# Optimization experiments

Measured on AMD Instinct MI355X. Metric: run time of the kernel, lower is better.

The kernel has to match this reference:

```python
import jax, jax.numpy as jnp
from jax import lax
import numpy as np

START = 1  # strings_utils.SpecialSymbol.START
B, T, H, V = 16, 256, 512, 32000


def setup_inputs() -> dict:
    key = jax.random.key(0)
    ks = jax.random.split(key, 8)
    s = 0.05
    return {
        "hidden0": jax.random.normal(ks[0], (1, B, H), jnp.float32),
        "target": jax.random.randint(ks[1], (B, T), 0, V, jnp.int32),
        "E": jax.random.normal(ks[2], (V, H), jnp.float32) * s,
        "W_ih": jax.random.normal(ks[3], (3 * H, H), jnp.float32) * s,
        "W_hh": jax.random.normal(ks[4], (3 * H, H), jnp.float32) * s,
        "b_ih": jax.random.normal(ks[5], (3 * H,), jnp.float32) * s,
        "b_hh": jax.random.normal(ks[6], (3 * H,), jnp.float32) * s,
        "b_out": jax.random.normal(ks[7], (V,), jnp.float32) * s,
    }


def reference(hidden0, target, E, W_ih, W_hh, b_ih, b_hh, b_out):
    # Teacher forcing: step 0 feeds START, step di>0 feeds target[:, di-1]
    b, t = target.shape
    start = jnp.full((b, 1), START, dtype=target.dtype)
    step_tok = jnp.concatenate([start, target[:, :-1]], axis=1).T  # [T, B]
    h0 = hidden0[0]  # num_layers == 1 -> [B, H]

    def step(h, tok):
        x = E[tok]                                # [B, H] embedding gather
        gi = x @ W_ih.T + b_ih                    # [B, 3H]
        gh = h @ W_hh.T + b_hh                    # [B, 3H]
        i_r, i_z, i_n = jnp.split(gi, 3, axis=-1)
        h_r, h_z, h_n = jnp.split(gh, 3, axis=-1)
        r = jax.nn.sigmoid(i_r + h_r)
        z = jax.nn.sigmoid(i_z + h_z)
        n = jnp.tanh(i_n + r * h_n)
        h_new = (1.0 - z) * n + z * h             # [B, H]
        logits = h_new @ E.T + b_out              # tied-weight output [B, V]
        return h_new, logits

    _, logits = lax.scan(step, h0, step_tok)      # [T, B, V]
    return jnp.transpose(logits, (1, 0, 2))       # [B, T, V]
```

## Files before the change

### kernel.cpp

```cpp
#include <hip/hip_runtime.h>
#include <hip/hip_bf16.h>
#include <math.h>

#define Bq 16
#define Tq 256
#define Hq 512
#define Vq 32000
#define Gq 1536
#define NWG 16
#define LBLK 240
#define NBI 167
#define NTILES (32 * NBI)

typedef __attribute__((ext_vector_type(8))) short short8;
typedef __attribute__((ext_vector_type(4))) float f32x4;
typedef __attribute__((ext_vector_type(4))) unsigned int u32x4;
typedef unsigned long long u64;

typedef const __attribute__((address_space(1))) void g_void;
typedef __attribute__((address_space(3))) void l_void;

__device__ __forceinline__ unsigned short f2bf(float f) {
    union { float f; unsigned int u; } v; v.f = f;
    unsigned int r = v.u + 0x7fffu + ((v.u >> 16) & 1u);
    return (unsigned short)(r >> 16);
}
__device__ __forceinline__ float bf2f(unsigned short h) {
    union { unsigned int u; float f; } v; v.u = ((unsigned int)h) << 16;
    return v.f;
}
__device__ __forceinline__ float sigm(float x) { return 1.0f / (1.0f + __expf(-x)); }
__device__ __forceinline__ float tanh_fast(float x) {
    float e = __expf(-2.0f * x);
    return (1.0f - e) / (1.0f + e);
}

__launch_bounds__(384)
__global__ void prep_gi_kernel(const int* __restrict__ target, const float* __restrict__ E,
                               const float* __restrict__ Wih, const float* __restrict__ Whh,
                               const float* __restrict__ b_ih,
                               unsigned short* __restrict__ Ebf,
                               unsigned short* __restrict__ WhhHi,
                               unsigned short* __restrict__ WhhLo,
                               float* __restrict__ gi_all,
                               int* __restrict__ flags) {
    int bid = blockIdx.x, tid = threadIdx.x;
    if (bid >= 4096) {
        long g = (long)(bid - 4096) * 384 + tid;
        long stride = 1536L * 384;
        for (long i = g; i < (long)Vq * Hq; i += stride) Ebf[i] = f2bf(E[i]);
        for (long i = g; i < (long)Gq * Hq; i += stride) {
            float w = Whh[i]; unsigned short hi = f2bf(w);
            WhhHi[i] = hi; WhhLo[i] = f2bf(w - bf2f(hi));
        }
        if (g < 2048) flags[g] = 0;
        return;
    }
    __shared__ __align__(16) unsigned short Ahi[16][520];
    __shared__ __align__(16) unsigned short Alo[16][520];
    __shared__ int toks[16];
    int t = bid >> 4, gb = bid & 15;
    if (tid < 16) toks[tid] = (t == 0) ? 1 : target[tid * Tq + (t - 1)];
    __syncthreads();
    for (int idx = tid; idx < 16 * Hq; idx += 384) {
        int r = idx >> 9, k = idx & 511;
        float v = E[(long)toks[r] * Hq + k];
        unsigned short hi = f2bf(v);
        Ahi[r][k] = hi; Alo[r][k] = f2bf(v - bf2f(hi));
    }
    __syncthreads();
    int wave = tid >> 6, lane = tid & 63;
    int gcb = gb * 96 + wave * 16;
    int row = lane & 15, kg = (lane >> 4) * 8;
    const float* wrow = Wih + (long)(gcb + row) * Hq;
    f32x4 aHH = {0,0,0,0}, aHL = {0,0,0,0}, aLH = {0,0,0,0};
#pragma unroll
    for (int ks = 0; ks < 16; ++ks) {
        int k0 = ks * 32 + kg;
        short8 ah = *(const short8*)&Ahi[row][k0];
        short8 al = *(const short8*)&Alo[row][k0];
        f32x4 wa = *(const f32x4*)&wrow[k0];
        f32x4 wb = *(const f32x4*)&wrow[k0 + 4];
        short8 wh, wl;
#pragma unroll
        for (int e = 0; e < 4; ++e) {
            unsigned short hi = f2bf(wa[e]);
            wh[e] = (short)hi; wl[e] = (short)f2bf(wa[e] - bf2f(hi));
            hi = f2bf(wb[e]);
            wh[e + 4] = (short)hi; wl[e + 4] = (short)f2bf(wb[e] - bf2f(hi));
        }
        aHH = __builtin_amdgcn_mfma_f32_16x16x32_bf16(ah, wh, aHH, 0, 0, 0);
        aHL = __builtin_amdgcn_mfma_f32_16x16x32_bf16(ah, wl, aHL, 0, 0, 0);
        aLH = __builtin_amdgcn_mfma_f32_16x16x32_bf16(al, wh, aLH, 0, 0, 0);
    }
    int g = gcb + row;
    float bi = b_ih[g];
#pragma unroll
    for (int q = 0; q < 4; ++q) {
        int b = (lane >> 4) * 4 + q;
        gi_all[((long)(t * 16 + b)) * Gq + g] = aHH[q] + aHL[q] + aLH[q] + bi;
    }
}

__launch_bounds__(384, 1)
__global__ void fused_kernel(const float* __restrict__ h0,
                             const unsigned short* __restrict__ WhhHi,
                             const unsigned short* __restrict__ WhhLo,
                             const float* __restrict__ b_hh,
                             const float* __restrict__ gi_all,
                             unsigned int* Hpk, u64* ring,
                             int* flags,
                             const unsigned short* __restrict__ Ebf,
                             const float* __restrict__ b_out,
                             float* __restrict__ out) {
    __shared__ __align__(16) char smem[41984];
    int tid = threadIdx.x, lane = tid & 63;

    if (blockIdx.x < NWG) {
        __builtin_amdgcn_s_setprio(1);
        unsigned short (*Ahi)[520] = (unsigned short (*)[520])smem;
        float (*gbuf)[16][33] = (float (*)[16][33])(smem + 16640);
        int w = blockIdx.x;
        int wave = tid >> 6;
        int gate = wave >> 1;
        int gcol = gate * 512 + w * 32 + (wave & 1) * 16;
        int row = lane & 15, kg = (lane >> 4) * 8;
        const unsigned short* bhp = WhhHi + (long)(gcol + row) * Hq;
        const unsigned short* blp = WhhLo + (long)(gcol + row) * Hq;
        short8 Bh[16], Bl[16];
#pragma unroll
        for (int ks = 0; ks < 16; ++ks) {
            Bh[ks] = *(const short8*)&bhp[ks * 32 + kg];
            Bl[ks] = *(const short8*)&blp[ks * 32 + kg];
        }
        float bhh = b_hh[gcol + row];
        float gin[4];
#pragma unroll
        for (int q = 0; q < 4; ++q) {
            int b = (lane >> 4) * 4 + q;
            gin[q] = gi_all[(long)b * Gq + (gcol + row)];
        }
        for (int t = 0; t < Tq; ++t) {
            if (t == 0) {
                for (int idx = tid; idx < Bq * Hq; idx += 384)
                    Ahi[idx >> 9][idx & 511] = f2bf(h0[idx]);
            } else {
                const u64* src = ring + ((t - 1) & 1) * 4096;
                u64 vb[11];
                bool ok;
                int guard = 0;
                do {
#pragma unroll
                    for (int k = 0; k < 10; ++k)
                        vb[k] = __hip_atomic_load(&src[tid + k * 384], __ATOMIC_RELAXED,
                                                  __HIP_MEMORY_SCOPE_AGENT);
                    vb[10] = (tid < 256)
                        ? __hip_atomic_load(&src[3840 + tid], __ATOMIC_RELAXED,
                                            __HIP_MEMORY_SCOPE_AGENT)
                        : ((u64)(unsigned int)t << 32);
                    ok = true;
#pragma unroll
                    for (int k = 0; k < 11; ++k)
                        ok = ok && ((unsigned int)(vb[k] >> 32) == (unsigned int)t);
                    if (!ok) __builtin_amdgcn_s_sleep(1);
                } while (!ok && ++guard < (1 << 15));
#pragma unroll
                for (int k = 0; k < 10; ++k) {
                    int wv = tid + k * 384;
                    *(unsigned int*)&Ahi[wv >> 8][(wv & 255) * 2] = (unsigned int)vb[k];
                }
                if (tid < 256) {
                    int wv = 3840 + tid;
                    *(unsigned int*)&Ahi[wv >> 8][(wv & 255) * 2] = (unsigned int)vb[10];
                }
            }
            __syncthreads();
            f32x4 xH = {0,0,0,0}, xL = {0,0,0,0};
            f32x4 yH = {0,0,0,0}, yL = {0,0,0,0};
#pragma unroll
            for (int ks = 0; ks < 8; ++ks) {
                short8 ah = *(const short8*)&Ahi[row][ks * 32 + kg];
                xH = __builtin_amdgcn_mfma_f32_16x16x32_bf16(ah, Bh[ks], xH, 0, 0, 0);
                xL = __builtin_amdgcn_mfma_f32_16x16x32_bf16(ah, Bl[ks], xL, 0, 0, 0);
            }
#pragma unroll
            for (int ks = 8; ks < 16; ++ks) {
                short8 ah = *(const short8*)&Ahi[row][ks * 32 + kg];
                yH = __builtin_amdgcn_mfma_f32_16x16x32_bf16(ah, Bh[ks], yH, 0, 0, 0);
                yL = __builtin_amdgcn_mfma_f32_16x16x32_bf16(ah, Bl[ks], yL, 0, 0, 0);
            }
            int jj = (wave & 1) * 16 + row;
#pragma unroll
            for (int q = 0; q < 4; ++q) {
                int b = (lane >> 4) * 4 + q;
                float ghv = (xH[q] + yH[q]) + (xL[q] + yL[q]) + bhh;
                if (gate < 2) gbuf[gate][b][jj] = ghv + gin[q];
                else { gbuf[2][b][jj] = gin[q]; gbuf[3][b][jj] = ghv; }
            }
            __syncthreads();
            if (tid < 256) {
                int b = tid >> 4, jp = tid & 15;
                int j0 = jp * 2, j1 = j0 + 1;
                int jc0 = w * 32 + j0;
                float r0 = sigm(gbuf[0][b][j0]);
                float z0 = sigm(gbuf[1][b][j0]);
                float n0 = tanh_fast(gbuf[2][b][j0] + r0 * gbuf[3][b][j0]);
                float hn0 = (1.0f - z0) * n0 + z0 * bf2f(Ahi[b][jc0]);
                float r1 = sigm(gbuf[0][b][j1]);
                float z1 = sigm(gbuf[1][b][j1]);
                float n1 = tanh_fast(gbuf[2][b][j1] + r1 * gbuf[3][b][j1]);
                float hn1 = (1.0f - z1) * n1 + z1 * bf2f(Ahi[b][jc0 + 1]);
                unsigned int pk = (unsigned int)f2bf(hn0) |
                                  ((unsigned int)f2bf(hn1) << 16);
                long idx = b * 256 + w * 16 + jp;
                u64 word = ((u64)(unsigned int)(t + 1) << 32) | pk;
                __hip_atomic_store(&ring[(t & 1) * 4096 + idx], word,
                                   __ATOMIC_RELAXED, __HIP_MEMORY_SCOPE_AGENT);
                __hip_atomic_store(&Hpk[(long)t * 4096 + idx], pk,
                                   __ATOMIC_RELAXED, __HIP_MEMORY_SCOPE_AGENT);
                if ((t & 7) == 7) {
                    asm volatile("s_waitcnt vmcnt(0)" ::: "memory");
                    if (lane == 0)
                        __hip_atomic_store(&flags[(w * 4 + wave) * 32], t + 1,
                                           __ATOMIC_RELAXED, __HIP_MEMORY_SCOPE_AGENT);
                }
            }
            int tp = (t + 1 < Tq) ? (t + 1) : t;
#pragma unroll
            for (int q = 0; q < 4; ++q) {
                int b = (lane >> 4) * 4 + q;
                gin[q] = gi_all[((long)(tp * 16 + b)) * Gq + (gcol + row)];
            }
        }
    } else {
        unsigned short* As = (unsigned short*)smem;
        unsigned short* Bs = As + 128 * 64;
        int slot = blockIdx.x - NWG;
        int wid = tid >> 6;
        int wr = wid & 1, wc = wid >> 1;
        int fr = lane & 15, r7 = lane & 7, sb = lane >> 4;
        int rA = lane >> 3, slp = (lane & 7) ^ rA;
        for (int tile = slot; tile < NTILES; tile += LBLK) {
            int mt = tile / NBI, nbi = tile % NBI;
            int m0 = mt * 128, n0 = nbi * 192;
            if (tid < 64) {
                int need = (mt + 1) * 8;
                int guard = 0;
                while (guard < (1 << 18)) {
                    int fv = __hip_atomic_load(&flags[lane * 32], __ATOMIC_RELAXED,
                                               __HIP_MEMORY_SCOPE_AGENT);
                    if (__all(fv >= need)) break;
                    __builtin_amdgcn_s_sleep(127);
                    ++guard;
                }
            }
            __syncthreads();
            f32x4 acc[4][4] = {};
            const unsigned int* srcA = Hpk + (long)(mt * 8) * 4096;
            for (int kt = 0; kt < 8; ++kt) {
                if (kt) __syncthreads();
                int ko = kt * 64;
#pragma unroll
                for (int i = 0; i < 4; ++i) {
                    int brow = n0 + wid * 8 + i * 48 + rA;
                    if (brow > Vq - 1) brow = Vq - 1;
                    __builtin_amdgcn_global_load_lds(
                        (g_void*)(Ebf + (long)brow * Hq + ko + slp * 8),
                        (l_void*)(Bs + (wid * 8 + i * 48) * 64), 16, 0, 0);
                }
                for (int c = tid; c < 1024; c += 384) {
                    int r = c >> 3, g8 = c & 7;
                    u32x4 v = *(const u32x4*)&srcA[(long)(r >> 4) * 4096 +
                                                   (r & 15) * 256 + kt * 32 + g8 * 4];
                    *(u32x4*)&As[r * 64 + ((g8 ^ (r & 7)) << 3)] = v;
                }
                __syncthreads();
#pragma unroll
                for (int ks = 0; ks < 2; ++ks) {
                    short8 af[4], bfr[4];
#pragma unroll
                    for (int f = 0; f < 4; ++f) {
                        af[f]  = *(const short8*)&As[(wr * 64 + f * 16 + fr) * 64 +
                                                     (((sb + ks * 4) ^ r7) << 3)];
                        bfr[f] = *(const short8*)&Bs[(wc * 64 + f * 16 + fr) * 64 +
                                                     (((sb + ks * 4) ^ r7) << 3)];
                    }
#pragma unroll
                    for (int fm = 0; fm < 4; ++fm)
#pragma unroll
                        for (int fn = 0; fn < 4; ++fn)
                            acc[fm][fn] = __builtin_amdgcn_mfma_f32_16x16x32_bf16(
                                af[fm], bfr[fn], acc[fm][fn], 0, 0, 0);
                }
            }
#pragma unroll
            for (int fn = 0; fn < 4; ++fn) {
                int v = n0 + wc * 64 + fn * 16 + fr;
                if (v < Vq) {
                    float bo = b_out[v];
#pragma unroll
                    for (int fm = 0; fm < 4; ++fm) {
#pragma unroll
                        for (int q = 0; q < 4; ++q) {
                            int m = m0 + wr * 64 + fm * 16 + (lane >> 4) * 4 + q;
                            out[((long)(m & 15) * Tq + (m >> 4)) * Vq + v] =
                                acc[fm][fn][q] + bo;
                        }
                    }
                }
            }
        }
    }
}

extern "C" void kernel_launch(void* const* d_in, const int* in_sizes, int n_in,
                              void* d_out, int out_size, void* d_ws, size_t ws_size,
                              hipStream_t stream) {
    const float* h0    = (const float*)d_in[0];
    const int*   target= (const int*)d_in[1];
    const float* E     = (const float*)d_in[2];
    const float* Wih   = (const float*)d_in[3];
    const float* Whh   = (const float*)d_in[4];
    const float* b_ih  = (const float*)d_in[5];
    const float* b_hh  = (const float*)d_in[6];
    const float* b_out = (const float*)d_in[7];
    float* out = (float*)d_out;

    char* ws = (char*)d_ws;
    size_t off = 0;
    unsigned short* Ebf   = (unsigned short*)(ws + off); off += (size_t)Vq * Hq * 2;
    unsigned short* WhhHi = (unsigned short*)(ws + off); off += (size_t)Gq * Hq * 2;
    unsigned short* WhhLo = (unsigned short*)(ws + off); off += (size_t)Gq * Hq * 2;
    float*          gi_all= (float*)(ws + off);          off += (size_t)Tq * Bq * Gq * 4;
    unsigned int*   Hpk   = (unsigned int*)(ws + off);   off += (size_t)Tq * 4096 * 4;
    u64*            ring  = (u64*)(ws + off);            off += (size_t)2 * 4096 * 8;
    int*            flags = (int*)(ws + off);            off += 2048 * 4;

    prep_gi_kernel<<<dim3(5632), dim3(384), 0, stream>>>(target, E, Wih, Whh, b_ih,
                                                         Ebf, WhhHi, WhhLo, gi_all,
                                                         flags);
    fused_kernel<<<dim3(256), dim3(384), 0, stream>>>(h0, WhhHi, WhhLo, b_hh, gi_all,
                                                      Hpk, ring, flags, Ebf, b_out, out);
}
```

Measured before the change: 926.4 us.

## Pre-split W_ih into bf16 hi/lo once and tighten ring polling with inline asm

Splits the combined prep/gi kernel in two. The new prep kernel converts W_ih into bf16 hi/lo arrays once, so the gi kernel loads pre-split bf16 weights instead of re-converting fp32 W_ih in every one of its 4096 blocks. This adds an extra kernel launch and serialises the gi computation after the conversion pass. Separately, the recurrent ring-buffer poll now uses inline-asm global_load_dwordx2 with sc0 sc1 cache bits and a single s_waitcnt, plus a wave-level __all vote, to cut spin-loop latency on the serial critical path.

```diff
diff --git a/kernel.cpp b/kernel.cpp
--- a/kernel.cpp
+++ b/kernel.cpp
@@ -35,31 +35,34 @@
     return (1.0f - e) / (1.0f + e);
 }
 
+__global__ void prep_kernel(const float* __restrict__ E, const float* __restrict__ Wih,
+                            const float* __restrict__ Whh,
+                            unsigned short* __restrict__ Ebf,
+                            unsigned short* __restrict__ WihHi, unsigned short* __restrict__ WihLo,
+                            unsigned short* __restrict__ WhhHi, unsigned short* __restrict__ WhhLo,
+                            int* __restrict__ flags) {
+    long tid = (long)blockIdx.x * blockDim.x + threadIdx.x;
+    long stride = (long)gridDim.x * blockDim.x;
+    for (long i = tid; i < (long)Vq * Hq; i += stride) Ebf[i] = f2bf(E[i]);
+    for (long i = tid; i < (long)Gq * Hq; i += stride) {
+        float w = Wih[i]; unsigned short hi = f2bf(w);
+        WihHi[i] = hi; WihLo[i] = f2bf(w - bf2f(hi));
+        w = Whh[i]; hi = f2bf(w);
+        WhhHi[i] = hi; WhhLo[i] = f2bf(w - bf2f(hi));
+    }
+    if (tid < 2048) flags[tid] = 0;
+}
+
 __launch_bounds__(384)
-__global__ void prep_gi_kernel(const int* __restrict__ target, const float* __restrict__ E,
-                               const float* __restrict__ Wih, const float* __restrict__ Whh,
-                               const float* __restrict__ b_ih,
-                               unsigned short* __restrict__ Ebf,
-                               unsigned short* __restrict__ WhhHi,
-                               unsigned short* __restrict__ WhhLo,
-                               float* __restrict__ gi_all,
-                               int* __restrict__ flags) {
-    int bid = blockIdx.x, tid = threadIdx.x;
-    if (bid >= 4096) {
-        long g = (long)(bid - 4096) * 384 + tid;
-        long stride = 1536L * 384;
-        for (long i = g; i < (long)Vq * Hq; i += stride) Ebf[i] = f2bf(E[i]);
-        for (long i = g; i < (long)Gq * Hq; i += stride) {
-            float w = Whh[i]; unsigned short hi = f2bf(w);
-            WhhHi[i] = hi; WhhLo[i] = f2bf(w - bf2f(hi));
-        }
-        if (g < 2048) flags[g] = 0;
-        return;
-    }
+__global__ void gi_kernel(const int* __restrict__ target, const float* __restrict__ E,
+                          const unsigned short* __restrict__ WihHi,
+                          const unsigned short* __restrict__ WihLo,
+                          const float* __restrict__ b_ih, float* __restrict__ gi_all) {
     __shared__ __align__(16) unsigned short Ahi[16][520];
     __shared__ __align__(16) unsigned short Alo[16][520];
     __shared__ int toks[16];
-    int t = bid >> 4, gb = bid & 15;
+    int t = blockIdx.x, gb = blockIdx.y;
+    int tid = threadIdx.x;
     if (tid < 16) toks[tid] = (t == 0) ? 1 : target[tid * Tq + (t - 1)];
     __syncthreads();
     for (int idx = tid; idx < 16 * Hq; idx += 384) {
@@ -72,23 +75,16 @@
     int wave = tid >> 6, lane = tid & 63;
     int gcb = gb * 96 + wave * 16;
     int row = lane & 15, kg = (lane >> 4) * 8;
-    const float* wrow = Wih + (long)(gcb + row) * Hq;
+    const unsigned short* bh = WihHi + (long)(gcb + row) * Hq;
+    const unsigned short* bl = WihLo + (long)(gcb + row) * Hq;
     f32x4 aHH = {0,0,0,0}, aHL = {0,0,0,0}, aLH = {0,0,0,0};
 #pragma unroll
     for (int ks = 0; ks < 16; ++ks) {
         int k0 = ks * 32 + kg;
         short8 ah = *(const short8*)&Ahi[row][k0];
         short8 al = *(const short8*)&Alo[row][k0];
-        f32x4 wa = *(const f32x4*)&wrow[k0];
-        f32x4 wb = *(const f32x4*)&wrow[k0 + 4];
-        short8 wh, wl;
-#pragma unroll
-        for (int e = 0; e < 4; ++e) {
-            unsigned short hi = f2bf(wa[e]);
-            wh[e] = (short)hi; wl[e] = (short)f2bf(wa[e] - bf2f(hi));
-            hi = f2bf(wb[e]);
-            wh[e + 4] = (short)hi; wl[e + 4] = (short)f2bf(wb[e] - bf2f(hi));
-        }
+        short8 wh = *(const short8*)&bh[k0];
+        short8 wl = *(const short8*)&bl[k0];
         aHH = __builtin_amdgcn_mfma_f32_16x16x32_bf16(ah, wh, aHH, 0, 0, 0);
         aHL = __builtin_amdgcn_mfma_f32_16x16x32_bf16(ah, wl, aHL, 0, 0, 0);
         aLH = __builtin_amdgcn_mfma_f32_16x16x32_bf16(al, wh, aLH, 0, 0, 0);
@@ -146,32 +142,80 @@
                     Ahi[idx >> 9][idx & 511] = f2bf(h0[idx]);
             } else {
                 const u64* src = ring + ((t - 1) & 1) * 4096;
-                u64 vb[11];
+                u64 A0 = (u64)(src + tid);
+                u64 A1 = (u64)(src + tid + 384);
+                u64 A2 = (u64)(src + tid + 768);
+                u64 A3 = (u64)(src + tid + 1152);
+                u64 A4 = (u64)(src + tid + 1536);
+                u64 A5 = (u64)(src + tid + 1920);
+                u64 A6 = (u64)(src + tid + 2304);
+                u64 A7 = (u64)(src + tid + 2688);
+                u64 A8 = (u64)(src + tid + 3072);
+                u64 A9 = (u64)(src + tid + 3456);
+                u64 A10 = (u64)(src + ((tid < 256) ? (3840 + tid) : tid));
+                u64 v0, v1, v2, v3, v4, v5, v6, v7, v8, v9, v10;
+                unsigned int st = (unsigned int)t;
+                int guard = 0;
                 bool ok;
-                int guard = 0;
                 do {
-#pragma unroll
-                    for (int k = 0; k < 10; ++k)
-                        vb[k] = __hip_atomic_load(&src[tid + k * 384], __ATOMIC_RELAXED,
-                                                  __HIP_MEMORY_SCOPE_AGENT);
-                    vb[10] = (tid < 256)
-                        ? __hip_atomic_load(&src[3840 + tid], __ATOMIC_RELAXED,
-                                            __HIP_MEMORY_SCOPE_AGENT)
-                        : ((u64)(unsigned int)t << 32);
-                    ok = true;
-#pragma unroll
-                    for (int k = 0; k < 11; ++k)
-                        ok = ok && ((unsigned int)(vb[k] >> 32) == (unsigned int)t);
+                    asm volatile(
+                        "global_load_dwordx2 %0, %11, off sc0 sc1\n\t"
+                        "global_load_dwordx2 %1, %12, off sc0 sc1\n\t"
+                        "global_load_dwordx2 %2, %13, off sc0 sc1\n\t"
+                        "global_load_dwordx2 %3, %14, off sc0 sc1\n\t"
+                        "global_load_dwordx2 %4, %15, off sc0 sc1\n\t"
+                        "global_load_dwordx2 %5, %16, off sc0 sc1\n\t"
+                        "global_load_dwordx2 %6, %17, off sc0 sc1\n\t"
+                        "global_load_dwordx2 %7, %18, off sc0 sc1\n\t"
+                        "global_load_dwordx2 %8, %19, off sc0 sc1\n\t"
+                        "global_load_dwordx2 %9, %20, off sc0 sc1\n\t"
+                        "global_load_dwordx2 %10, %21, off sc0 sc1\n\t"
+                        "s_waitcnt vmcnt(0)"
+                        : "=&v"(v0), "=&v"(v1), "=&v"(v2), "=&v"(v3), "=&v"(v4),
+                          "=&v"(v5), "=&v"(v6), "=&v"(v7), "=&v"(v8), "=&v"(v9),
+                          "=&v"(v10)
+                        : "v"(A0), "v"(A1), "v"(A2), "v"(A3), "v"(A4), "v"(A5),
+                          "v"(A6), "v"(A7), "v"(A8), "v"(A9), "v"(A10)
+                        : "memory");
+                    bool mine = ((unsigned int)(v0 >> 32) == st) &&
+                                ((unsigned int)(v1 >> 32) == st) &&
+                                ((unsigned int)(v2 >> 32) == st) &&
+                                ((unsigned int)(v3 >> 32) == st) &&
+                                ((unsigned int)(v4 >> 32) == st) &&
+                                ((unsigned int)(v5 >> 32) == st) &&
+                                ((unsigned int)(v6 >> 32) == st) &&
+                                ((unsigned int)(v7 >> 32) == st) &&
+                                ((unsigned int)(v8 >> 32) == st) &&
+                                ((unsigned int)(v9 >> 32) == st) &&
+                                ((unsigned int)(v10 >> 32) == st);
+                    ok = __all(mine);
                     if (!ok) __builtin_amdgcn_s_sleep(1);
                 } while (!ok && ++guard < (1 << 15));
-#pragma unroll
-                for (int k = 0; k < 10; ++k) {
-                    int wv = tid + k * 384;
-                    *(unsigned int*)&Ahi[wv >> 8][(wv & 255) * 2] = (unsigned int)vb[k];
-                }
-                if (tid < 256) {
-                    int wv = 3840 + tid;
-                    *(unsigned int*)&Ahi[wv >> 8][(wv & 255) * 2] = (unsigned int)vb[10];
+                {
+                    int wv = tid;
+                    *(unsigned int*)&Ahi[wv >> 8][(wv & 255) * 2] = (unsigned int)v0;
+                    wv = tid + 384;
+                    *(unsigned int*)&Ahi[wv >> 8][(wv & 255) * 2] = (unsigned int)v1;
+                    wv = tid + 768;
+                    *(unsigned int*)&Ahi[wv >> 8][(wv & 255) * 2] = (unsigned int)v2;
+                    wv = tid + 1152;
+                    *(unsigned int*)&Ahi[wv >> 8][(wv & 255) * 2] = (unsigned int)v3;
+                    wv = tid + 1536;
+                    *(unsigned int*)&Ahi[wv >> 8][(wv & 255) * 2] = (unsigned int)v4;
+                    wv = tid + 1920;
+                    *(unsigned int*)&Ahi[wv >> 8][(wv & 255) * 2] = (unsigned int)v5;
+                    wv = tid + 2304;
+                    *(unsigned int*)&Ahi[wv >> 8][(wv & 255) * 2] = (unsigned int)v6;
+                    wv = tid + 2688;
+                    *(unsigned int*)&Ahi[wv >> 8][(wv & 255) * 2] = (unsigned int)v7;
+                    wv = tid + 3072;
+                    *(unsigned int*)&Ahi[wv >> 8][(wv & 255) * 2] = (unsigned int)v8;
+                    wv = tid + 3456;
+                    *(unsigned int*)&Ahi[wv >> 8][(wv & 255) * 2] = (unsigned int)v9;
+                    if (tid < 256) {
+                        wv = 3840 + tid;
+                        *(unsigned int*)&Ahi[wv >> 8][(wv & 255) * 2] = (unsigned int)v10;
+                    }
                 }
             }
             __syncthreads();
@@ -329,6 +373,8 @@
     char* ws = (char*)d_ws;
     size_t off = 0;
     unsigned short* Ebf   = (unsigned short*)(ws + off); off += (size_t)Vq * Hq * 2;
+    unsigned short* WihHi = (unsigned short*)(ws + off); off += (size_t)Gq * Hq * 2;
+    unsigned short* WihLo = (unsigned short*)(ws + off); off += (size_t)Gq * Hq * 2;
     unsigned short* WhhHi = (unsigned short*)(ws + off); off += (size_t)Gq * Hq * 2;
     unsigned short* WhhLo = (unsigned short*)(ws + off); off += (size_t)Gq * Hq * 2;
     float*          gi_all= (float*)(ws + off);          off += (size_t)Tq * Bq * Gq * 4;
@@ -336,9 +382,9 @@
     u64*            ring  = (u64*)(ws + off);            off += (size_t)2 * 4096 * 8;
     int*            flags = (int*)(ws + off);            off += 2048 * 4;
 
-    prep_gi_kernel<<<dim3(5632), dim3(384), 0, stream>>>(target, E, Wih, Whh, b_ih,
-                                                         Ebf, WhhHi, WhhLo, gi_all,
-                                                         flags);
+    prep_kernel<<<dim3(2048), dim3(256), 0, stream>>>(E, Wih, Whh, Ebf, WihHi, WihLo,
+                                                      WhhHi, WhhLo, flags);
+    gi_kernel<<<dim3(Tq, 16), dim3(384), 0, stream>>>(target, E, WihHi, WihLo, b_ih, gi_all);
     fused_kernel<<<dim3(256), dim3(384), 0, stream>>>(h0, WhhHi, WhhLo, b_hh, gi_all,
                                                       Hpk, ring, flags, Ebf, b_out, out);
 }
```

New measurement: 927.8 us. No clear change (+0.2%).
